# Kernel tuning notes

Measured on AMD Instinct MI355X. Metric: run time of the kernel, lower is better.

The kernel has to match this reference:

```python
import jax, jax.numpy as jnp
import numpy as np

ALPHA, GAMMA = 0.8, 2.0
EDGE_W, BOUND_W, CE_W, POS_W = 1.0, 1.0, 1.0, 1.0


def setup_inputs() -> dict:
    key = jax.random.key(0)
    k1, k2 = jax.random.split(key)
    B, C, H, W = 16, 1, 256, 256
    inputs = jax.random.normal(k1, (B, C, H, W), dtype=jnp.float32)
    # binary GT mask (scipy EDT path assumes a {0,1} mask)
    targets = (jax.random.uniform(k2, (B, C, H, W)) < 0.3).astype(jnp.float32)
    return {"inputs": inputs, "targets": targets}


def _edt_sq(seed):
    """Exact squared Euclidean distance transform of a (H,W) bool grid.
    seed==True pixels have distance 0 (i.e. zeros of scipy's input).
    Separable brute-force: d2(x,y) = min_j [ min_i (f(i,j)+(x-i)^2) + (y-j)^2 ]."""
    H, W = seed.shape
    INF = jnp.float32(H * H + W * W)
    f = jnp.where(seed, 0.0, INF)                              # (H,W)
    ih = jnp.arange(H, dtype=jnp.float32)
    dh = (ih[:, None] - ih[None, :]) ** 2                      # (H,H)
    g = jnp.min(f[None, :, :] + dh[:, :, None], axis=1)       # (H,W)
    iw = jnp.arange(W, dtype=jnp.float32)
    dw = (iw[:, None] - iw[None, :]) ** 2                      # (W,W)
    return jnp.min(g[:, :, None] + dw[None, :, :], axis=1)    # (H,W)


def _compute_sdf(gt):
    """gt: (B,1,H,W) binary. Signed distance: edt(~pos) - edt(pos); 0 if no pos."""
    pos = gt[:, 0] > 0.5                                        # (B,H,W)
    d_out = jnp.sqrt(jax.vmap(_edt_sq)(~pos))                   # dist to pos pixels
    d_in = jnp.sqrt(jax.vmap(_edt_sq)(pos))                     # dist to neg pixels
    sdf = d_out - d_in
    has_pos = jnp.any(pos, axis=(1, 2))[:, None, None]
    return jnp.where(has_pos, sdf, 0.0)[:, None]                # (B,1,H,W)


def _sobel_mag(x):
    """kornia.filters.Sobel: replicate pad, normalized sobel kernels (/8), magnitude."""
    kx = jnp.array([[-1., 0., 1.], [-2., 0., 2.], [-1., 0., 1.]], jnp.float32) / 8.0
    ky = kx.T
    k = jnp.stack([kx, ky])[:, None]                            # (2,1,3,3) OIHW
    xp = jnp.pad(x, ((0, 0), (0, 0), (1, 1), (1, 1)), mode='edge')
    g = jax.lax.conv_general_dilated(xp, k, (1, 1), 'VALID',
                                     dimension_numbers=('NCHW', 'OIHW', 'NCHW'))
    return jnp.sqrt(g[:, 0:1] ** 2 + g[:, 1:2] ** 2 + 1e-6)


def reference(inputs, targets):
    x, t = inputs, targets
    log_p = jax.nn.log_sigmoid(x)
    log_np = jax.nn.log_sigmoid(-x)

    # focal
    bce = -(t * log_p + (1.0 - t) * log_np)
    pt = jnp.exp(-bce)
    focal = jnp.mean(ALPHA * (1.0 - pt) ** GAMMA * bce)

    # edge (L1 on sobel magnitudes)
    edge = jnp.mean(jnp.abs(_sobel_mag(jax.nn.sigmoid(x)) - _sobel_mag(t)))

    # boundary: SDF is computed on CPU/numpy in torch -> non-differentiable constant
    sdf = jax.lax.stop_gradient(_compute_sdf(t))
    boundary = jnp.mean((jax.nn.sigmoid(x) - t) * sdf)

    # weighted BCE with logits (pos_weight)
    ce = jnp.mean(-(POS_W * t * log_p + (1.0 - t) * log_np))

    return focal + EDGE_W * edge + BOUND_W * boundary + CE_W * ce
```

## Files before the change

### kernel.cpp

```cpp
#include <hip/hip_runtime.h>
#include <math.h>

#define BB 16
#define HH 256
#define WW 256
#define NN (BB*HH*WW)
#define SCAN_INIT 300
#define BIGR 100000

static __device__ constexpr float INF_EDT = 131072.0f;

__device__ __forceinline__ float sigmoidf(float v){ return 1.0f/(1.0f+expf(-v)); }
__device__ __forceinline__ float logsigf(float v){
  return fminf(v, 0.0f) - log1pf(expf(-fabsf(v)));
}
__device__ __forceinline__ float min3f(float a, float b, float c){
  return fminf(fminf(a, b), c);
}

__global__ __launch_bounds__(512) void edt_cols_scan(const float* __restrict__ tgt,
                                                     float* __restrict__ gA,
                                                     float* __restrict__ gB,
                                                     int* __restrict__ hp_blk){
  __shared__ unsigned int fwd_s[HH*64];
  __shared__ int lastp_s[8][64], firstp_s[8][64];
  __shared__ int lastn_s[8][64], firstn_s[8][64];
  const int b  = blockIdx.x >> 2;
  const int j0 = (blockIdx.x & 3) << 6;
  const int w  = threadIdx.x >> 6;
  const int l  = threadIdx.x & 63;
  const int j  = j0 + l;
  const int r0 = w << 5;

  int dp = SCAN_INIT, dn = SCAN_INIT;
  int firstp = BIGR, lastp = -BIGR, firstn = BIGR, lastn = -BIGR;
  #pragma unroll 4
  for (int i = 0; i < 32; ++i){
    const int gi = r0 + i;
    const float tv = tgt[(b*HH + gi)*WW + j];
    const bool s = tv > 0.5f;
    dp = s ? 0 : dp + 1;
    dn = s ? dn + 1 : 0;
    if (s){ lastp = gi; if (firstp == BIGR) firstp = gi; }
    else  { lastn = gi; if (firstn == BIGR) firstn = gi; }
    fwd_s[gi*64 + l] = ((unsigned)dp << 16) | (unsigned)dn;
  }
  lastp_s[w][l] = lastp; firstp_s[w][l] = firstp;
  lastn_s[w][l] = lastn; firstn_s[w][l] = firstn;
  __syncthreads();

  int upP = -BIGR, dnP = BIGR, upN = -BIGR, dnN = BIGR;
  int allLastP = -BIGR, allLastN = -BIGR;
  #pragma unroll
  for (int s = 0; s < 8; ++s){
    const int lp = lastp_s[s][l], fp = firstp_s[s][l];
    const int ln = lastn_s[s][l], fn = firstn_s[s][l];
    allLastP = max(allLastP, lp); allLastN = max(allLastN, ln);
    if (s < w){ upP = max(upP, lp); upN = max(upN, ln); }
    if (s > w){ dnP = min(dnP, fp); dnN = min(dnN, fn); }
  }
  const bool colp = allLastP >= 0;
  const bool coln = allLastN >= 0;
  if (w == 0){
    unsigned long long bal = __ballot(colp);
    if (l == 0) hp_blk[blockIdx.x] = bal ? 1 : 0;
  }

  int bp = SCAN_INIT, bn = SCAN_INIT;
  #pragma unroll 4
  for (int i = 31; i >= 0; --i){
    const int gi = r0 + i;
    const unsigned f = fwd_s[gi*64 + l];
    const int fp = (int)(f >> 16), fn = (int)(f & 0xffffu);
    bp = (fp == 0) ? 0 : bp + 1;
    bn = (fn == 0) ? 0 : bn + 1;
    int Dp = min(min(fp, bp), min(gi - upP, dnP - gi));
    int Dn = min(min(fn, bn), min(gi - upN, dnN - gi));
    Dp = min(Dp, 512); Dn = min(Dn, 512);
    const int o = (b*HH + gi)*WW + j;
    gA[o] = colp ? (float)(Dp*Dp) : INF_EDT;
    gB[o] = coln ? (float)(Dn*Dn) : INF_EDT;
  }
}

__global__ __launch_bounds__(256) void fused_row_k(const float* __restrict__ inp,
    const float* __restrict__ tgt, const float* __restrict__ gA, const float* __restrict__ gB,
    const int* __restrict__ hp_blk, float* __restrict__ part){
  __shared__ __align__(16) float ga_s[4][WW];
  __shared__ __align__(16) float gb_s[4][WW];
  __shared__ __align__(16) float ss[6][WW];
  __shared__ __align__(16) float tt[6][WW];
  __shared__ float red[4];
  const int b  = blockIdx.x >> 6;
  const int x0 = (blockIdx.x & 63) << 2;
  const int t  = threadIdx.x;
  const int g = t >> 6, l = t & 63;

  {
    const int l4 = l << 2;
    const int base = (b*HH + x0 + g)*WW + l4;
    *(float4*)&ga_s[g][l4] = *(const float4*)&gA[base];
    *(float4*)&gb_s[g][l4] = *(const float4*)&gB[base];
    for (int k = g; k < 6; k += 4){
      int gr = x0 - 1 + k; gr = gr < 0 ? 0 : (gr > HH-1 ? HH-1 : gr);
      const float4 xv = *(const float4*)&inp[(b*HH + gr)*WW + l4];
      const float4 tv = *(const float4*)&tgt[(b*HH + gr)*WW + l4];
      float4 sv; sv.x = sigmoidf(xv.x); sv.y = sigmoidf(xv.y);
      sv.z = sigmoidf(xv.z); sv.w = sigmoidf(xv.w);
      *(float4*)&ss[k][l4] = sv;
      *(float4*)&tt[k][l4] = tv;
    }
  }
  __syncthreads();

  const int y = t;
  const int hp_ = hp_blk[4*b] | hp_blk[4*b+1] | hp_blk[4*b+2] | hp_blk[4*b+3];
  const int cm = y ? y-1 : 0, cp = y < WW-1 ? y+1 : WW-1;

  float a0m = ss[0][cm], a0c = ss[0][y], a0p = ss[0][cp];
  float a1m = ss[1][cm], a1c = ss[1][y], a1p = ss[1][cp];
  float b0m = tt[0][cm], b0c = tt[0][y], b0p = tt[0][cp];
  float b1m = tt[1][cm], b1c = tt[1][y], b1p = tt[1][cp];

  float acc = 0.0f;
  #pragma unroll
  for (int r = 0; r < 4; ++r){
    float dpv = ga_s[r][y];
    float dnv = gb_s[r][y];
    int wm = (int)sqrtf(fmaxf(dpv, dnv)) + 1; if (wm > 255) wm = 255;
    for (int dj = 1; dj <= wm; dj += 4){
      #pragma unroll
      for (int u = 0; u < 4; ++u){
        const int d = dj + u;
        const float d2 = (float)(d*d);
        const int jl = (y - d) < 0   ? 0   : y - d;
        const int jr = (y + d) > 255 ? 255 : y + d;
        dpv = min3f(dpv, ga_s[r][jl] + d2, ga_s[r][jr] + d2);
        dnv = min3f(dnv, gb_s[r][jl] + d2, gb_s[r][jr] + d2);
      }
    }
    const float a2m = ss[r+2][cm], a2c = ss[r+2][y], a2p = ss[r+2][cp];
    const float b2m = tt[r+2][cm], b2c = tt[r+2][y], b2p = tt[r+2][cp];
    const float gxs = ((a0p-a0m) + 2.0f*(a1p-a1m) + (a2p-a2m)) * 0.125f;
    const float gys = ((a2m-a0m) + 2.0f*(a2c-a0c) + (a2p-a0p)) * 0.125f;
    const float mags = sqrtf(gxs*gxs + gys*gys + 1e-6f);
    const float gxt = ((b0p-b0m) + 2.0f*(b1p-b1m) + (b2p-b2m)) * 0.125f;
    const float gyt = ((b2m-b0m) + 2.0f*(b2c-b0c) + (b2p-b0p)) * 0.125f;
    const float magt = sqrtf(gxt*gxt + gyt*gyt + 1e-6f);
    acc += fabsf(mags - magt);
    a0m=a1m; a0c=a1c; a0p=a1p; a1m=a2m; a1c=a2c; a1p=a2p;
    b0m=b1m; b0c=b1c; b0p=b1p; b1m=b2m; b1c=b2c; b1p=b2p;

    const float xv = inp[(b*HH + x0 + r)*WW + y];
    const float tv = tt[r+1][y];
    const float sg = ss[r+1][y];
    float sdf = sqrtf(dnv) - sqrtf(dpv);
    sdf = hp_ ? sdf : 0.0f;
    acc += (sg - tv) * sdf;
    const float lp = logsigf(xv);
    const float ln = logsigf(-xv);
    const float bce = -(tv*lp + (1.0f - tv)*ln);
    const float pt = expf(-bce);
    const float om = 1.0f - pt;
    acc += 0.8f * om * om * bce;
    acc += bce;
  }

  #pragma unroll
  for (int o = 32; o > 0; o >>= 1) acc += __shfl_down(acc, o);
  if (l == 0) red[g] = acc;
  __syncthreads();
  if (t == 0) part[blockIdx.x] = red[0]+red[1]+red[2]+red[3];
}

__global__ __launch_bounds__(256) void finalize_k(const float* __restrict__ part,
                                                  float* __restrict__ out){
  __shared__ float red[4];
  const int t = threadIdx.x;
  float s = 0.0f;
  #pragma unroll
  for (int i = t; i < 1024; i += 256) s += part[i];
  #pragma unroll
  for (int o = 32; o > 0; o >>= 1) s += __shfl_down(s, o);
  if ((t & 63) == 0) red[t >> 6] = s;
  __syncthreads();
  if (t == 0) out[0] = (red[0]+red[1]+red[2]+red[3]) * (1.0f/(float)NN);
}

extern "C" void kernel_launch(void* const* d_in, const int* in_sizes, int n_in,
                              void* d_out, int out_size, void* d_ws, size_t ws_size,
                              hipStream_t stream){
  const float* inp = (const float*)d_in[0];
  const float* tgt = (const float*)d_in[1];
  float* out = (float*)d_out;
  float* gA   = (float*)d_ws;
  float* gB   = gA + NN;
  float* part = gB + NN;
  int* hp_blk = (int*)(part + 1024);

  edt_cols_scan<<<BB*4, 512, 0, stream>>>(tgt, gA, gB, hp_blk);
  fused_row_k<<<BB*(HH/4), 256, 0, stream>>>(inp, tgt, gA, gB, hp_blk, part);
  finalize_k<<<1, 256, 0, stream>>>(part, out);
}
```

Baseline: 93.06 us.

## Repartition column EDT scan into 256 narrower blocks with shorter segments

Restructures the column-scan kernel from 64 blocks of 512 threads (64 columns × 8 segments of 32 rows) to 256 blocks of 256 threads (16 columns × 16 segments of 16 rows). The aim is more blocks to fill the GPU's compute units and shorter serial scans per thread. The cost is narrower 64-byte coalesced loads and stores per row and a longer cross-segment combine loop. The has-positive flag now ORs 16 per-block entries instead of 4.

```diff
diff --git a/kernel.cpp b/kernel.cpp
--- a/kernel.cpp
+++ b/kernel.cpp
@@ -18,24 +18,23 @@
   return fminf(fminf(a, b), c);
 }
 
-__global__ __launch_bounds__(512) void edt_cols_scan(const float* __restrict__ tgt,
+__global__ __launch_bounds__(256) void edt_cols_scan(const float* __restrict__ tgt,
                                                      float* __restrict__ gA,
                                                      float* __restrict__ gB,
                                                      int* __restrict__ hp_blk){
-  __shared__ unsigned int fwd_s[HH*64];
-  __shared__ int lastp_s[8][64], firstp_s[8][64];
-  __shared__ int lastn_s[8][64], firstn_s[8][64];
-  const int b  = blockIdx.x >> 2;
-  const int j0 = (blockIdx.x & 3) << 6;
-  const int w  = threadIdx.x >> 6;
-  const int l  = threadIdx.x & 63;
-  const int j  = j0 + l;
-  const int r0 = w << 5;
+  __shared__ unsigned int fwd_s[HH*16];
+  __shared__ int lastp_s[16*16], firstp_s[16*16];
+  __shared__ int lastn_s[16*16], firstn_s[16*16];
+  const int b   = blockIdx.x >> 4;
+  const int j0  = (blockIdx.x & 15) << 4;
+  const int t   = threadIdx.x;
+  const int col = t & 15, seg = t >> 4;
+  const int j = j0 + col, r0 = seg << 4;
 
   int dp = SCAN_INIT, dn = SCAN_INIT;
   int firstp = BIGR, lastp = -BIGR, firstn = BIGR, lastn = -BIGR;
   #pragma unroll 4
-  for (int i = 0; i < 32; ++i){
+  for (int i = 0; i < 16; ++i){
     const int gi = r0 + i;
     const float tv = tgt[(b*HH + gi)*WW + j];
     const bool s = tv > 0.5f;
@@ -43,34 +42,33 @@
     dn = s ? dn + 1 : 0;
     if (s){ lastp = gi; if (firstp == BIGR) firstp = gi; }
     else  { lastn = gi; if (firstn == BIGR) firstn = gi; }
-    fwd_s[gi*64 + l] = ((unsigned)dp << 16) | (unsigned)dn;
-  }
-  lastp_s[w][l] = lastp; firstp_s[w][l] = firstp;
-  lastn_s[w][l] = lastn; firstn_s[w][l] = firstn;
-  __syncthreads();
-
-  int upP = -BIGR, dnP = BIGR, upN = -BIGR, dnN = BIGR;
-  int allLastP = -BIGR, allLastN = -BIGR;
-  #pragma unroll
-  for (int s = 0; s < 8; ++s){
-    const int lp = lastp_s[s][l], fp = firstp_s[s][l];
-    const int ln = lastn_s[s][l], fn = firstn_s[s][l];
-    allLastP = max(allLastP, lp); allLastN = max(allLastN, ln);
-    if (s < w){ upP = max(upP, lp); upN = max(upN, ln); }
-    if (s > w){ dnP = min(dnP, fp); dnN = min(dnN, fn); }
-  }
-  const bool colp = allLastP >= 0;
-  const bool coln = allLastN >= 0;
-  if (w == 0){
+    fwd_s[gi*16 + col] = ((unsigned)dp << 16) | (unsigned)dn;
+  }
+  lastp_s[seg*16+col] = lastp; firstp_s[seg*16+col] = firstp;
+  lastn_s[seg*16+col] = lastn; firstn_s[seg*16+col] = firstn;
+  __syncthreads();
+
+  int upP=-BIGR, dnP=BIGR, upN=-BIGR, dnN=BIGR, allP=-BIGR, allN=-BIGR;
+  #pragma unroll
+  for (int s2 = 0; s2 < 16; ++s2){
+    const int lp = lastp_s[s2*16+col], fp = firstp_s[s2*16+col];
+    const int ln = lastn_s[s2*16+col], fn = firstn_s[s2*16+col];
+    allP = max(allP, lp); allN = max(allN, ln);
+    if (s2 < seg){ upP = max(upP, lp); upN = max(upN, ln); }
+    if (s2 > seg){ dnP = min(dnP, fp); dnN = min(dnN, fn); }
+  }
+  const bool colp = allP >= 0;
+  const bool coln = allN >= 0;
+  if (t < 64){
     unsigned long long bal = __ballot(colp);
-    if (l == 0) hp_blk[blockIdx.x] = bal ? 1 : 0;
+    if (t == 0) hp_blk[blockIdx.x] = bal ? 1 : 0;
   }
 
   int bp = SCAN_INIT, bn = SCAN_INIT;
   #pragma unroll 4
-  for (int i = 31; i >= 0; --i){
+  for (int i = 15; i >= 0; --i){
     const int gi = r0 + i;
-    const unsigned f = fwd_s[gi*64 + l];
+    const unsigned f = fwd_s[gi*16 + col];
     const int fp = (int)(f >> 16), fn = (int)(f & 0xffffu);
     bp = (fp == 0) ? 0 : bp + 1;
     bn = (fn == 0) ? 0 : bn + 1;
@@ -113,8 +111,11 @@
   }
   __syncthreads();
 
+  int hp_ = 0;
+  #pragma unroll
+  for (int i = 0; i < 16; ++i) hp_ |= hp_blk[b*16 + i];
+
   const int y = t;
-  const int hp_ = hp_blk[4*b] | hp_blk[4*b+1] | hp_blk[4*b+2] | hp_blk[4*b+3];
   const int cm = y ? y-1 : 0, cp = y < WW-1 ? y+1 : WW-1;
 
   float a0m = ss[0][cm], a0c = ss[0][y], a0p = ss[0][cp];
@@ -198,7 +199,7 @@
   float* part = gB + NN;
   int* hp_blk = (int*)(part + 1024);
 
-  edt_cols_scan<<<BB*4, 512, 0, stream>>>(tgt, gA, gB, hp_blk);
+  edt_cols_scan<<<BB*16, 256, 0, stream>>>(tgt, gA, gB, hp_blk);
   fused_row_k<<<BB*(HH/4), 256, 0, stream>>>(inp, tgt, gA, gB, hp_blk, part);
   finalize_k<<<1, 256, 0, stream>>>(part, out);
 }
```

Result: faster. 86.32 us (-7.2%).
